# Kernel optimization log

Measured on AMD Instinct MI355X. Metric: run time of the kernel, lower is better.

## Reference

```python
import jax, jax.numpy as jnp
import numpy as np

N = 50000      # nodes
E = 1_600_000  # edges (avg degree 32)
IN, H, OUT, R = 128, 64, 32, 8
NEG_SLOPE = 0.2


def _rgat(x, src, dst, etype, W, q, k, b, n_nodes):
    """PyG RGATConv, defaults: heads=1, dim=1, additive-self-attention,
    across-relation softmax, concat=True, bias=True, dropout=0 (eval)."""
    # per-relation transform of all nodes: [R, N, O] (cheaper than per-edge bmm since 2*deg >> R)
    t = jnp.einsum('ni,rio->rno', x, W)
    xi = t[etype, dst]                      # [E, O] transformed target feats
    xj = t[etype, src]                      # [E, O] transformed source feats
    a = (xi @ q + xj @ k)[:, 0]             # [E] additive attention logits
    a = jnp.where(a >= 0, a, NEG_SLOPE * a)  # leaky_relu
    # segment softmax over incoming edges of each target node (across relations)
    m = jax.ops.segment_max(a, dst, num_segments=n_nodes)
    m = jnp.where(jnp.isfinite(m), m, 0.0)
    ex = jnp.exp(a - m[dst])
    s = jax.ops.segment_sum(ex, dst, num_segments=n_nodes)
    alpha = ex / (s[dst] + 1e-16)
    out = jax.ops.segment_sum(alpha[:, None] * xj, dst, num_segments=n_nodes)
    return out + b


def setup_inputs() -> dict:
    key = jax.random.key(0)
    ks = jax.random.split(key, 24)
    x = jax.random.normal(ks[0], (N, IN), jnp.float32)
    edge_index = jax.random.randint(ks[1], (2, E), 0, N, jnp.int32)
    edge_type = jax.random.randint(ks[2], (E,), 0, R, jnp.int32)

    def glorot(k, shape, fan_in):
        return jax.random.normal(k, shape, jnp.float32) * (1.0 / np.sqrt(fan_in))

    d = dict(x=x, edge_index=edge_index, edge_type=edge_type)
    # conv1: in->hidden, conv_mu / conv_logvar: hidden->hidden
    d['W1'] = glorot(ks[3], (R, IN, H), IN)
    d['q1'] = glorot(ks[4], (H, 1), H)
    d['k1'] = glorot(ks[5], (H, 1), H)
    d['b1'] = jnp.zeros((H,), jnp.float32)
    d['Wmu'] = glorot(ks[6], (R, H, H), H)
    d['qmu'] = glorot(ks[7], (H, 1), H)
    d['kmu'] = glorot(ks[8], (H, 1), H)
    d['bmu'] = jnp.zeros((H,), jnp.float32)
    d['Wlv'] = glorot(ks[9], (R, H, H), H)
    d['qlv'] = glorot(ks[10], (H, 1), H)
    d['klv'] = glorot(ks[11], (H, 1), H)
    d['blv'] = jnp.zeros((H,), jnp.float32)
    d['Wm'] = glorot(ks[12], (H, OUT), H)   # linear_mu (stored [in,out])
    d['bm'] = jnp.zeros((OUT,), jnp.float32)
    d['Wl'] = glorot(ks[13], (H, OUT), H)   # linear_logvar
    d['bl'] = jnp.zeros((OUT,), jnp.float32)
    return d


def reference(x, edge_index, edge_type, W1, q1, k1, b1,
              Wmu, qmu, kmu, bmu, Wlv, qlv, klv, blv, Wm, bm, Wl, bl):
    src, dst = edge_index[0], edge_index[1]
    hidden = jax.nn.relu(_rgat(x, src, dst, edge_type, W1, q1, k1, b1, N))
    mu = jax.nn.relu(_rgat(hidden, src, dst, edge_type, Wmu, qmu, kmu, bmu, N))
    mu = mu @ Wm + bm                       # dropout is identity in eval
    logvar = jax.nn.relu(_rgat(hidden, src, dst, edge_type, Wlv, qlv, klv, blv, N))
    logvar = logvar @ Wl + bl
    logstd = 0.5 * logvar
    return (mu, logstd)
```

## Files before the change

kernel.cpp:

```cpp
#include <hip/hip_runtime.h>
#include <cstdint>

#define HDIM 64
#define ODIM 32
#define NEG_SLOPE 0.2f
#define SCHUNK 2048
#define EPB 8192

typedef __attribute__((ext_vector_type(8))) short v8s;
typedef __attribute__((ext_vector_type(4))) float v4f;

__device__ __forceinline__ unsigned f2bf_rne(float f) {
  unsigned u = __float_as_uint(f);
  return (u + 0x7FFFu + ((u >> 16) & 1u)) >> 16;
}

__device__ __forceinline__ unsigned fenc(float f) {
  unsigned u = __float_as_uint(f);
  return (u & 0x80000000u) ? ~u : (u | 0x80000000u);
}
__device__ __forceinline__ float fdec(unsigned e) {
  unsigned u = (e & 0x80000000u) ? (e ^ 0x80000000u) : ~e;
  return __uint_as_float(u);
}

__global__ __launch_bounds__(256) void cvt_bf16_kernel(
    const float* __restrict__ in, unsigned short* __restrict__ out, int n) {
  int i = (blockIdx.x * 256 + threadIdx.x) * 4;
  if (i + 3 < n) {
    float4 v = *(const float4*)&in[i];
    ushort4 o;
    o.x = (unsigned short)f2bf_rne(v.x);
    o.y = (unsigned short)f2bf_rne(v.y);
    o.z = (unsigned short)f2bf_rne(v.z);
    o.w = (unsigned short)f2bf_rne(v.w);
    *(ushort4*)&out[i] = o;
  }
}

__global__ __launch_bounds__(256) void transpose_w_kernel(
    const float* __restrict__ W1, const float* __restrict__ Wmu,
    const float* __restrict__ Wlv, unsigned short* __restrict__ W1t,
    unsigned short* __restrict__ Wct) {
  const int b = blockIdx.x;
  if (b < 8) {
    const int r = b;
    for (int idx = threadIdx.x; idx < 128 * 64; idx += 256) {
      const int kk = idx >> 6, o = idx & 63;
      W1t[((size_t)r * 64 + o) * 128 + kk] =
          (unsigned short)f2bf_rne(W1[((size_t)r * 128 + kk) * 64 + o]);
    }
  } else {
    const int s = (b - 8) >> 3, r = (b - 8) & 7;
    const float* src = s ? Wlv : Wmu;
    for (int idx = threadIdx.x; idx < 64 * 64; idx += 256) {
      const int kk = idx >> 6, o = idx & 63;
      Wct[((size_t)s * 64 + o) * 512 + r * 64 + kk] =
          (unsigned short)f2bf_rne(src[((size_t)r * 64 + kk) * 64 + o]);
    }
  }
}

__global__ __launch_bounds__(256) void prep_T_kernel(
    const float* __restrict__ Wmu, const float* __restrict__ qmu,
    const float* __restrict__ kmu, const float* __restrict__ Wlv,
    const float* __restrict__ qlv, const float* __restrict__ klv,
    float* __restrict__ T) {
  for (int idx = threadIdx.x; idx < 2048; idx += 256) {
    const int j = idx >> 6, c = idx & 63;
    const int isk = j >> 4, sr = j & 15, s = sr >> 3, r = sr & 7;
    const float* W = s ? Wlv : Wmu;
    const float* vec = s ? (isk ? klv : qlv) : (isk ? kmu : qmu);
    float acc = 0.f;
    for (int o = 0; o < 64; o++)
      acc += W[((size_t)r * 64 + c) * 64 + o] * vec[o];
    T[idx] = acc;
  }
}

__global__ __launch_bounds__(256) void count_deg_kernel(
    const int* __restrict__ dst, const int* __restrict__ etype,
    int* __restrict__ deg, int E) {
  int e = blockIdx.x * 256 + threadIdx.x;
  if (e < E) atomicAdd(&deg[dst[e] * 8 + etype[e]], 1);
}

__global__ __launch_bounds__(256) void scan_p1(const int* __restrict__ deg,
                                               int* __restrict__ bsum, int n) {
  int base = blockIdx.x * SCHUNK + threadIdx.x * 8;
  int s = 0;
#pragma unroll
  for (int j = 0; j < 8; j++) {
    int i = base + j;
    if (i < n) s += deg[i];
  }
#pragma unroll
  for (int d = 1; d < 64; d <<= 1) s += __shfl_xor(s, d, 64);
  __shared__ int ws[4];
  if ((threadIdx.x & 63) == 0) ws[threadIdx.x >> 6] = s;
  __syncthreads();
  if (threadIdx.x == 0) bsum[blockIdx.x] = ws[0] + ws[1] + ws[2] + ws[3];
}

__global__ __launch_bounds__(256) void scan_p2(int* bsum, int nb) {
  __shared__ int wsum[4];
  const int i = threadIdx.x;
  int v = (i < nb) ? bsum[i] : 0;
  const int orig = v;
  const int lane = i & 63, w = i >> 6;
#pragma unroll
  for (int d = 1; d < 64; d <<= 1) {
    int up = __shfl_up(v, d, 64);
    if (lane >= d) v += up;
  }
  if (lane == 63) wsum[w] = v;
  __syncthreads();
  int woff = 0;
#pragma unroll
  for (int k = 0; k < 4; k++) woff += (k < w) ? wsum[k] : 0;
  if (i < nb) bsum[i] = woff + v - orig;
}

__global__ __launch_bounds__(256) void scan_p3(const int* __restrict__ deg,
                                               const int* __restrict__ bsum,
                                               int* __restrict__ row_ptr,
                                               int n) {
  int base = blockIdx.x * SCHUNK + threadIdx.x * 8;
  int vals[8];
  int s = 0;
#pragma unroll
  for (int j = 0; j < 8; j++) {
    int i = base + j;
    vals[j] = (i < n) ? deg[i] : 0;
    s += vals[j];
  }
  int lane = threadIdx.x & 63, w = threadIdx.x >> 6;
  int v = s;
#pragma unroll
  for (int d = 1; d < 64; d <<= 1) {
    int up = __shfl_up(v, d, 64);
    if (lane >= d) v += up;
  }
  __shared__ int wsum[4];
  if (lane == 63) wsum[w] = v;
  __syncthreads();
  int woff = 0;
#pragma unroll
  for (int i = 0; i < 4; i++) woff += (i < w) ? wsum[i] : 0;
  int off = bsum[blockIdx.x] + woff + v - s;
#pragma unroll
  for (int j = 0; j < 8; j++) {
    int i = base + j;
    off += vals[j];
    if (i < n) row_ptr[i + 1] = off;
  }
  if (blockIdx.x == 0 && threadIdx.x == 0) row_ptr[0] = 0;
}

__global__ __launch_bounds__(256) void bucket_cursor_init(
    const int* __restrict__ rp2, int* __restrict__ cursor, int N, int nb) {
  int i = threadIdx.x;
  if (i < nb) cursor[i] = rp2[(size_t)min(i * 256, N) * 8];
}

__global__ __launch_bounds__(256) void bucket_pass1(
    const int* __restrict__ src, const int* __restrict__ dst,
    const int* __restrict__ etype, int* __restrict__ cursor,
    unsigned* __restrict__ tmp, int E) {
  __shared__ int hist[256];
  __shared__ int binstart[256];
  __shared__ int gbase[256];
  __shared__ int fill[256];
  __shared__ int wsum[4];
  __shared__ unsigned stage[EPB];
  __shared__ unsigned char binof[EPB];
  const int tid = threadIdx.x;
  const int e0 = blockIdx.x * EPB;
  const int cnt = min(EPB, E - e0);

  hist[tid] = 0;
  fill[tid] = 0;
  __syncthreads();
  for (int j = tid; j < cnt; j += 256) atomicAdd(&hist[dst[e0 + j] >> 8], 1);
  __syncthreads();

  const int hv = hist[tid];
  {
    const int lane = tid & 63, w = tid >> 6;
    int iv = hv;
#pragma unroll
    for (int d = 1; d < 64; d <<= 1) {
      int up = __shfl_up(iv, d, 64);
      if (lane >= d) iv += up;
    }
    if (lane == 63) wsum[w] = iv;
    __syncthreads();
    int woff = 0;
#pragma unroll
    for (int i = 0; i < 4; i++) woff += (i < w) ? wsum[i] : 0;
    binstart[tid] = woff + iv - hv;
    if (hv > 0) gbase[tid] = atomicAdd(&cursor[tid], hv);
  }
  __syncthreads();

  for (int j = tid; j < cnt; j += 256) {
    const int d = dst[e0 + j];
    const int b = d >> 8;
    const unsigned rec = ((unsigned)(d & 255) << 19) |
                         ((unsigned)etype[e0 + j] << 16) |
                         (unsigned)src[e0 + j];
    const int slot = binstart[b] + atomicAdd(&fill[b], 1);
    stage[slot] = rec;
    binof[slot] = (unsigned char)b;
  }
  __syncthreads();

  for (int s = tid; s < cnt; s += 256) {
    const int b = binof[s];
    tmp[gbase[b] + (s - binstart[b])] = stage[s];
  }
}

__global__ __launch_bounds__(256) void bucket_pass2(
    const int* __restrict__ rp2, const unsigned* __restrict__ tmp,
    int* __restrict__ edges, int N) {
  __shared__ int rp[2049];
  __shared__ int fill[2048];
  const int tid = threadIdx.x;
  const int rowbase = blockIdx.x * 256;
  const int rowcnt = min(256, N - rowbase);
  for (int i = tid; i <= rowcnt * 8; i += 256) rp[i] = rp2[(size_t)rowbase * 8 + i];
  for (int i = tid; i < 2048; i += 256) fill[i] = 0;
  __syncthreads();
  const int beg = rp[0];
  const int endv = rp[rowcnt * 8];
  for (int i = beg + tid; i < endv; i += 256) {
    const unsigned rec = tmp[i];
    const int bin = rec >> 16;
    const int pos = rp[bin] + atomicAdd(&fill[bin], 1);
    edges[pos] = (int)(rec & 0x7FFFFu);
  }
}

__global__ __launch_bounds__(256) void rowmax_kernel(
    const float* __restrict__ ak, unsigned* __restrict__ maxk_enc, int N) {
  const int row = blockIdx.x;
  const int nchunks = gridDim.y;
  const int per = (N + nchunks - 1) / nchunks;
  const int beg = blockIdx.y * per;
  const int end = min(N, beg + per);
  const float* r = ak + (size_t)row * N;
  float m = -1e30f;
  for (int i = beg + threadIdx.x; i < end; i += 256) m = fmaxf(m, r[i]);
#pragma unroll
  for (int d = 1; d < 64; d <<= 1) m = fmaxf(m, __shfl_xor(m, d, 64));
  __shared__ float ws[4];
  if ((threadIdx.x & 63) == 0) ws[threadIdx.x >> 6] = m;
  __syncthreads();
  if (threadIdx.x == 0) {
    float bm = fmaxf(fmaxf(ws[0], ws[1]), fmaxf(ws[2], ws[3]));
    atomicMax(&maxk_enc[row], fenc(bm));
  }
}

__global__ __launch_bounds__(256) void transform1_mfma(
    const unsigned short* __restrict__ xb,
    const unsigned short* __restrict__ W1t, const float* __restrict__ q,
    const float* __restrict__ k, unsigned short* __restrict__ tb,
    float* __restrict__ aq, float* __restrict__ ak, int N) {
  __shared__ unsigned short st[4][16][72];
  const int r = blockIdx.x;
  const int tid = threadIdx.x;
  const int w = tid >> 6;
  const int lane = tid & 63;
  const int quad = lane >> 4;
  const int mrow = lane & 15;
  const int n0w = blockIdx.y * 64 + w * 16;

  const int gA = min(n0w + mrow, N - 1);
  const unsigned short* arow = xb + (size_t)gA * 128 + quad * 8;
  const unsigned short* wrow = W1t + ((size_t)r * 64 + mrow) * 128 + quad * 8;

  v4f acc[4];
#pragma unroll
  for (int tt = 0; tt < 4; tt++) acc[tt] = (v4f){0.f, 0.f, 0.f, 0.f};

#pragma unroll
  for (int k0 = 0; k0 < 128; k0 += 32) {
    v8s a = *(const v8s*)(arow + k0);
#pragma unroll
    for (int tt = 0; tt < 4; tt++) {
      v8s b = *(const v8s*)(wrow + (size_t)tt * 16 * 128 + k0);
      acc[tt] = __builtin_amdgcn_mfma_f32_16x16x32_bf16(a, b, acc[tt], 0, 0, 0);
    }
  }

  float qv[4], kv[4];
#pragma unroll
  for (int tt = 0; tt < 4; tt++) {
    qv[tt] = q[tt * 16 + mrow];
    kv[tt] = k[tt * 16 + mrow];
  }

#pragma unroll
  for (int i = 0; i < 4; i++) {
    float vq = 0.f, vk = 0.f;
#pragma unroll
    for (int tt = 0; tt < 4; tt++) {
      vq = fmaf(acc[tt][i], qv[tt], vq);
      vk = fmaf(acc[tt][i], kv[tt], vk);
      st[w][quad * 4 + i][tt * 16 + mrow] =
          (unsigned short)f2bf_rne(acc[tt][i]);
    }
#pragma unroll
    for (int d = 1; d < 16; d <<= 1) {
      vq += __shfl_xor(vq, d, 64);
      vk += __shfl_xor(vk, d, 64);
    }
    const int gn = n0w + quad * 4 + i;
    if (mrow == 0 && gn < N) {
      aq[(size_t)r * N + gn] = vq;
      ak[(size_t)r * N + gn] = vk;
    }
  }
  __syncthreads();

  const int row = lane >> 2, cg = lane & 3;
  const int gns = n0w + row;
  if (gns < N) {
    const uint4 v0 = *(const uint4*)&st[w][row][cg * 16];
    const uint4 v1 = *(const uint4*)&st[w][row][cg * 16 + 8];
    uint4* dst = (uint4*)&tb[((size_t)r * N + gns) * 64 + cg * 16];
    dst[0] = v0;
    dst[1] = v1;
  }
}

__global__ __launch_bounds__(256) void aggregate_kernel(
    const int* __restrict__ rp2, const int* __restrict__ edges,
    const unsigned short* __restrict__ tb, const float* __restrict__ aq,
    const float* __restrict__ ak, const unsigned* __restrict__ maxk_enc,
    const float* __restrict__ bias, unsigned short* __restrict__ hb, int N) {
  const int tid = threadIdx.x;
  const int w = tid >> 6, o = tid & 63;
  int wid = blockIdx.x * 4 + w;
  const bool valid = wid < N;
  if (!valid) wid = N - 1;
  const int beg = rp2[(size_t)wid * 8];
  const int end = valid ? rp2[(size_t)wid * 8 + 8] : beg;
  const int deg = end - beg;

  const float aqw = aq[(size_t)(o & 7) * N + wid];

  float v = aqw + fdec(maxk_enc[o & 7]);
  v = (v >= 0.f) ? v : NEG_SLOPE * v;
#pragma unroll
  for (int d = 1; d < 8; d <<= 1) v = fmaxf(v, __shfl_xor(v, d, 64));
  const float m = __shfl(v, 0, 64);

  const int g = o >> 3;
  const int cl = o & 7;
  float s = 0.f;
  float acc[8];
#pragma unroll
  for (int c = 0; c < 8; c++) acc[c] = 0.f;

  for (int base = 0; base < deg; base += 64) {
    const int j = base + o;
    const int gcount = min(64, deg - base);
    const int packed = edges[beg + min(j, deg - 1)];
    const int src = packed & 0xFFFF;
    const int rr = packed >> 16;
    const int idx = rr * N + src;
    float x = __shfl(aqw, rr, 64) + ak[idx];
    x = (x >= 0.f) ? x : NEG_SLOPE * x;
    const float p = (j < deg) ? __expf(x - m) : 0.f;
    s += p;
    const int g8 = (gcount + 7) & ~7;
    for (int u = 0; u < g8; u += 8) {
      const int e = u + g;
      const float pe = __shfl(p, e, 64);
      const int ie = __shfl(idx, e, 64);
      const uint4 tv = *(const uint4*)(tb + (size_t)ie * 64 + cl * 8);
      const unsigned uu0 = tv.x, uu1 = tv.y, uu2 = tv.z, uu3 = tv.w;
      acc[0] = fmaf(pe, __uint_as_float(uu0 << 16), acc[0]);
      acc[1] = fmaf(pe, __uint_as_float(uu0 & 0xFFFF0000u), acc[1]);
      acc[2] = fmaf(pe, __uint_as_float(uu1 << 16), acc[2]);
      acc[3] = fmaf(pe, __uint_as_float(uu1 & 0xFFFF0000u), acc[3]);
      acc[4] = fmaf(pe, __uint_as_float(uu2 << 16), acc[4]);
      acc[5] = fmaf(pe, __uint_as_float(uu2 & 0xFFFF0000u), acc[5]);
      acc[6] = fmaf(pe, __uint_as_float(uu3 << 16), acc[6]);
      acc[7] = fmaf(pe, __uint_as_float(uu3 & 0xFFFF0000u), acc[7]);
    }
  }
#pragma unroll
  for (int d = 1; d < 64; d <<= 1) s += __shfl_xor(s, d, 64);
#pragma unroll
  for (int d = 8; d < 64; d <<= 1) {
#pragma unroll
    for (int c = 0; c < 8; c++) acc[c] += __shfl_xor(acc[c], d, 64);
  }

  if (valid && g == 0) {
    const float inv = 1.f / (s + 1e-16f);
    unsigned rv[8];
#pragma unroll
    for (int c = 0; c < 8; c++) {
      const float res = acc[c] * inv + bias[cl * 8 + c];
      rv[c] = f2bf_rne(fmaxf(res, 0.f));
    }
    uint4 pkd;
    pkd.x = rv[0] | (rv[1] << 16);
    pkd.y = rv[2] | (rv[3] << 16);
    pkd.z = rv[4] | (rv[5] << 16);
    pkd.w = rv[6] | (rv[7] << 16);
    *(uint4*)(hb + (size_t)wid * 64 + cl * 8) = pkd;
  }
}

__global__ __launch_bounds__(256) void logit2_kernel(
    const unsigned short* __restrict__ hb, const float* __restrict__ T,
    float* __restrict__ aq2, float* __restrict__ ak2, int N) {
  __shared__ float Ts[2048];
  for (int i = threadIdx.x; i < 2048; i += 256) Ts[i] = T[i];
  __syncthreads();
  const int n = blockIdx.x * 256 + threadIdx.x;
  if (n >= N) return;
  float h[64];
  const unsigned short* hr = hb + (size_t)n * 64;
#pragma unroll
  for (int d = 0; d < 8; d++) {
    const uint4 u = *(const uint4*)(hr + d * 8);
    h[d * 8 + 0] = __uint_as_float(u.x << 16);
    h[d * 8 + 1] = __uint_as_float(u.x & 0xFFFF0000u);
    h[d * 8 + 2] = __uint_as_float(u.y << 16);
    h[d * 8 + 3] = __uint_as_float(u.y & 0xFFFF0000u);
    h[d * 8 + 4] = __uint_as_float(u.z << 16);
    h[d * 8 + 5] = __uint_as_float(u.z & 0xFFFF0000u);
    h[d * 8 + 6] = __uint_as_float(u.w << 16);
    h[d * 8 + 7] = __uint_as_float(u.w & 0xFFFF0000u);
  }
#pragma unroll
  for (int j = 0; j < 16; j++) {
    float dq = 0.f, dk = 0.f;
#pragma unroll
    for (int c = 0; c < 64; c++) {
      dq = fmaf(h[c], Ts[j * 64 + c], dq);
      dk = fmaf(h[c], Ts[(16 + j) * 64 + c], dk);
    }
    aq2[(size_t)j * N + n] = dq;
    ak2[(size_t)j * N + n] = dk;
  }
}

__global__ __launch_bounds__(256) void aggregate2h_kernel(
    const int* __restrict__ rp2, const int* __restrict__ edges,
    const unsigned short* __restrict__ hb, const float* __restrict__ aq2,
    const float* __restrict__ ak2, const unsigned* __restrict__ maxk2_enc,
    unsigned* __restrict__ y, float* __restrict__ sbuf, int N) {
  __shared__ float sred[2][2];
  const int tid = threadIdx.x;
  const int w = tid >> 6, o = tid & 63;
  const int nl = w >> 1;
  const int rbase = (w & 1) * 4;
  int wid = blockIdx.x * 2 + nl;
  const bool valid = wid < N;
  if (!valid) wid = N - 1;
  if (tid < 4) ((float*)sred)[tid] = 0.f;
  __syncthreads();

  const float aqw = aq2[(size_t)(o & 15) * N + wid];
  float v = aqw + fdec(maxk2_enc[o & 15]);
  v = (v >= 0.f) ? v : NEG_SLOPE * v;
#pragma unroll
  for (int d = 1; d < 8; d <<= 1) v = fmaxf(v, __shfl_xor(v, d, 64));
  const float m0 = __shfl(v, 0, 64);
  const float m1 = __shfl(v, 8, 64);

  const int g = o >> 5;
  const int k = o & 31;
  float s0 = 0.f, s1 = 0.f;
  float aE0[4], aO0[4], aE1[4], aO1[4];
#pragma unroll
  for (int r = 0; r < 4; r++) {
    aE0[r] = 0.f;
    aO0[r] = 0.f;
    aE1[r] = 0.f;
    aO1[r] = 0.f;
  }

  const size_t segbase = (size_t)wid * 8 + rbase;
#pragma unroll
  for (int r = 0; r < 4; r++) {
    const int sb = rp2[segbase + r];
    const int se = rp2[segbase + r + 1];
    if (valid && sb < se) {
      const float aqr0 = __shfl(aqw, rbase + r, 64);
      const float aqr1 = __shfl(aqw, 8 + rbase + r, 64);
      for (int base = sb; base < se; base += 64) {
        const int j = base + o;
        const int cnt = min(64, se - base);
        const int src = edges[min(j, se - 1)] & 0xFFFF;
        const float akv0 = ak2[(size_t)(rbase + r) * N + src];
        const float akv1 = ak2[(size_t)(8 + rbase + r) * N + src];
        float x0 = aqr0 + akv0;
        float x1 = aqr1 + akv1;
        x0 = (x0 >= 0.f) ? x0 : NEG_SLOPE * x0;
        x1 = (x1 >= 0.f) ? x1 : NEG_SLOPE * x1;
        const float p0 = (j < se) ? __expf(x0 - m0) : 0.f;
        const float p1 = (j < se) ? __expf(x1 - m1) : 0.f;
        s0 += p0;
        s1 += p1;
        for (int u = 0; 2 * u < cnt; u++) {
          const int e = 2 * u + g;
          const float pe0 = __shfl(p0, e, 64);
          const float pe1 = __shfl(p1, e, 64);
          const int ie = __shfl(src, e, 64);
          const unsigned hw =
              *(const unsigned*)(hb + (size_t)ie * 64 + k * 2);
          const float h0 = __uint_as_float(hw << 16);
          const float h1 = __uint_as_float(hw & 0xFFFF0000u);
          aE0[r] = fmaf(pe0, h0, aE0[r]);
          aO0[r] = fmaf(pe0, h1, aO0[r]);
          aE1[r] = fmaf(pe1, h0, aE1[r]);
          aO1[r] = fmaf(pe1, h1, aO1[r]);
        }
      }
    }
  }

#pragma unroll
  for (int d = 1; d < 64; d <<= 1) {
    s0 += __shfl_xor(s0, d, 64);
    s1 += __shfl_xor(s1, d, 64);
  }
#pragma unroll
  for (int r = 0; r < 4; r++) {
    aE0[r] += __shfl_xor(aE0[r], 32, 64);
    aO0[r] += __shfl_xor(aO0[r], 32, 64);
    aE1[r] += __shfl_xor(aE1[r], 32, 64);
    aO1[r] += __shfl_xor(aO1[r], 32, 64);
  }
  if (valid && o == 0) {
    atomicAdd(&sred[nl][0], s0);
    atomicAdd(&sred[nl][1], s1);
  }
  if (valid && g == 0) {
#pragma unroll
    for (int r = 0; r < 4; r++) {
      const unsigned u0 = f2bf_rne(aE0[r]) | (f2bf_rne(aO0[r]) << 16);
      const unsigned u1 = f2bf_rne(aE1[r]) | (f2bf_rne(aO1[r]) << 16);
      y[(size_t)wid * 256 + (rbase + r) * 32 + k] = u0;
      y[((size_t)N + wid) * 256 + (rbase + r) * 32 + k] = u1;
    }
  }
  __syncthreads();
  if (valid && o == 0 && rbase == 0) {
    sbuf[(size_t)wid * 2 + 0] = sred[nl][0];
    sbuf[(size_t)wid * 2 + 1] = sred[nl][1];
  }
}

__global__ __launch_bounds__(256) void out2_kernel(
    const unsigned short* __restrict__ yb,
    const unsigned short* __restrict__ Wct, const float* __restrict__ sbuf,
    const float* __restrict__ bmu, const float* __restrict__ blv,
    const float* __restrict__ Wm, const float* __restrict__ bm,
    const float* __restrict__ Wl, const float* __restrict__ bl,
    float* __restrict__ out_mu, float* __restrict__ out_ls, int N) {
  __shared__ float hstf[64][65];
  __shared__ float WL[2048];
  __shared__ float b2L[32];
  const int s = blockIdx.y;
  const int tid = threadIdx.x;
  for (int i = tid; i < 2048; i += 256) WL[i] = s ? Wl[i] : Wm[i];
  if (tid < 32) b2L[tid] = s ? bl[tid] : bm[tid];

  const int w = tid >> 6, lane = tid & 63;
  const int quad = lane >> 4, mrow = lane & 15;
  const int n0w = blockIdx.x * 64 + w * 16;
  const int gA = min(n0w + mrow, N - 1);
  const unsigned short* arow = yb + ((size_t)s * N + gA) * 512 + quad * 8;
  const unsigned short* wrow = Wct + ((size_t)s * 64 + mrow) * 512 + quad * 8;

  v4f acc[4];
#pragma unroll
  for (int tt = 0; tt < 4; tt++) acc[tt] = (v4f){0.f, 0.f, 0.f, 0.f};
#pragma unroll
  for (int k0 = 0; k0 < 512; k0 += 32) {
    v8s a = *(const v8s*)(arow + k0);
#pragma unroll
    for (int tt = 0; tt < 4; tt++) {
      v8s b = *(const v8s*)(wrow + (size_t)tt * 16 * 512 + k0);
      acc[tt] = __builtin_amdgcn_mfma_f32_16x16x32_bf16(a, b, acc[tt], 0, 0, 0);
    }
  }

  const float* bc = s ? blv : bmu;
#pragma unroll
  for (int i = 0; i < 4; i++) {
    const int node = min(n0w + quad * 4 + i, N - 1);
    const float inv = 1.f / (sbuf[(size_t)node * 2 + s] + 1e-16f);
#pragma unroll
    for (int tt = 0; tt < 4; tt++) {
      hstf[w * 16 + quad * 4 + i][tt * 16 + mrow] =
          fmaxf(acc[tt][i] * inv + bc[tt * 16 + mrow], 0.f);
    }
  }
  __syncthreads();

  const float mul = s ? 0.5f : 1.f;
  float* outp = s ? out_ls : out_mu;
  for (int idx = tid; idx < 2048; idx += 256) {
    const int nl2 = idx >> 5, oo = idx & 31;
    const int node = blockIdx.x * 64 + nl2;
    float a2 = 0.f;
#pragma unroll
    for (int c = 0; c < 64; c++) a2 = fmaf(hstf[nl2][c], WL[c * 32 + oo], a2);
    if (node < N) outp[(size_t)node * 32 + oo] = (a2 + b2L[oo]) * mul;
  }
}

extern "C" void kernel_launch(void* const* d_in, const int* in_sizes, int n_in,
                              void* d_out, int out_size, void* d_ws,
                              size_t ws_size, hipStream_t stream) {
  const float* x = (const float*)d_in[0];
  const int* edge_index = (const int*)d_in[1];
  const int* edge_type = (const int*)d_in[2];
  const float* W1 = (const float*)d_in[3];
  const float* q1 = (const float*)d_in[4];
  const float* k1 = (const float*)d_in[5];
  const float* b1 = (const float*)d_in[6];
  const float* Wmu = (const float*)d_in[7];
  const float* qmu = (const float*)d_in[8];
  const float* kmu = (const float*)d_in[9];
  const float* bmu = (const float*)d_in[10];
  const float* Wlv = (const float*)d_in[11];
  const float* qlv = (const float*)d_in[12];
  const float* klv = (const float*)d_in[13];
  const float* blv = (const float*)d_in[14];
  const float* Wm = (const float*)d_in[15];
  const float* bm = (const float*)d_in[16];
  const float* Wl = (const float*)d_in[17];
  const float* bl = (const float*)d_in[18];

  const int N = in_sizes[0] / 128;
  const int E = in_sizes[2];
  const int R = in_sizes[3] / (128 * 64);

  float* out_mu = (float*)d_out;
  float* out_ls = (float*)d_out + (size_t)N * ODIM;

  char* wsp = (char*)d_ws;
  size_t off = 0;
  auto carve = [&](size_t bytes) {
    void* p = wsp + off;
    off += (bytes + 255) & ~(size_t)255;
    return p;
  };

  void* tbuf = carve((size_t)R * N * 64 * sizeof(unsigned));
  unsigned short* t1b = (unsigned short*)tbuf;
  unsigned short* yb = (unsigned short*)tbuf;
  unsigned* yw = (unsigned*)tbuf;
  unsigned short* xb = (unsigned short*)carve((size_t)N * 128 * 2);
  unsigned short* hb = (unsigned short*)carve((size_t)N * 64 * 2);
  unsigned short* W1t = (unsigned short*)carve((size_t)R * 64 * 128 * 2);
  unsigned short* Wct = (unsigned short*)carve((size_t)2 * 64 * 512 * 2);
  float* Tdir = (float*)carve((size_t)32 * 64 * sizeof(float));
  float* aq2 = (float*)carve((size_t)2 * R * N * sizeof(float));
  float* ak2 = (float*)carve((size_t)2 * R * N * sizeof(float));
  unsigned* maxk_enc = (unsigned*)carve(2 * R * sizeof(unsigned));
  float* sbuf = (float*)carve((size_t)N * 2 * sizeof(float));
  int* deg = (int*)carve((size_t)N * 8 * sizeof(int));
  int* rp2 = (int*)carve(((size_t)N * 8 + 1) * sizeof(int));
  int* bsum = (int*)carve(256 * sizeof(int));
  int* cursor = (int*)carve(256 * sizeof(int));
  unsigned* tmp = (unsigned*)carve((size_t)E * sizeof(unsigned));
  int* edges = (int*)carve((size_t)E * sizeof(int));

  const int* e_src = edge_index;
  const int* e_dst = edge_index + E;

  cvt_bf16_kernel<<<(N * 128 / 4 + 255) / 256, 256, 0, stream>>>(x, xb,
                                                                 N * 128);
  transpose_w_kernel<<<24, 256, 0, stream>>>(W1, Wmu, Wlv, W1t, Wct);
  prep_T_kernel<<<1, 256, 0, stream>>>(Wmu, qmu, kmu, Wlv, qlv, klv, Tdir);

  hipMemsetAsync(deg, 0, (size_t)N * 8 * sizeof(int), stream);
  hipMemsetAsync(maxk_enc, 0, 2 * R * sizeof(unsigned), stream);
  count_deg_kernel<<<(E + 255) / 256, 256, 0, stream>>>(e_dst, edge_type, deg,
                                                        E);
  const int n2 = N * 8;
  const int nchunk = (n2 + SCHUNK - 1) / SCHUNK;
  scan_p1<<<nchunk, 256, 0, stream>>>(deg, bsum, n2);
  scan_p2<<<1, 256, 0, stream>>>(bsum, nchunk);
  scan_p3<<<nchunk, 256, 0, stream>>>(deg, bsum, rp2, n2);

  const int nbuck = (N + 255) >> 8;
  bucket_cursor_init<<<1, 256, 0, stream>>>(rp2, cursor, N, nbuck);
  bucket_pass1<<<(E + EPB - 1) / EPB, 256, 0, stream>>>(e_src, e_dst,
                                                        edge_type, cursor,
                                                        tmp, E);
  bucket_pass2<<<nbuck, 256, 0, stream>>>(rp2, tmp, edges, N);

  const int nb64 = (N + 63) / 64;

  transform1_mfma<<<dim3(R, nb64), 256, 0, stream>>>(xb, W1t, q1, k1, t1b,
                                                     aq2, ak2, N);
  rowmax_kernel<<<dim3(R, 32), 256, 0, stream>>>(ak2, maxk_enc, N);
  aggregate_kernel<<<(N + 3) / 4, 256, 0, stream>>>(rp2, edges, t1b, aq2, ak2,
                                                    maxk_enc, b1, hb, N);

  logit2_kernel<<<(N + 255) / 256, 256, 0, stream>>>(hb, Tdir, aq2, ak2, N);
  hipMemsetAsync(maxk_enc, 0, 2 * R * sizeof(unsigned), stream);
  rowmax_kernel<<<dim3(2 * R, 32), 256, 0, stream>>>(ak2, maxk_enc, N);
  aggregate2h_kernel<<<(N + 1) / 2, 256, 0, stream>>>(rp2, edges, hb, aq2,
                                                      ak2, maxk_enc, yw, sbuf,
                                                      N);
  out2_kernel<<<dim3(nb64, 2), 256, 0, stream>>>(yb, Wct, sbuf, bmu, blv, Wm,
                                                 bm, Wl, bl, out_mu, out_ls,
                                                 N);
}
```

Measured before the change: 609.4 us.

## Fuse per-relation key max into producers and restructure layer-2 aggregation per relation

Removes the two rowmax kernels and one memset by computing the per-relation max of key logits inside transform1 and logit2, combined across blocks with atomicMax on an encoded float. The layer-2 aggregation is rewritten so each wave handles one node, with 8 lanes per relation segment walking edges serially. Each lane loads 16 bytes of the source row and keeps 8-wide accumulators, which replaces the old shuffle-broadcast loop and the shared-memory reduction. The serial per-segment loop exposes load latency per edge and leaves lanes idle when relation degrees are uneven, in exchange for fewer shuffles, no block syncs and wider loads.

```diff
diff --git a/kernel.cpp b/kernel.cpp
--- a/kernel.cpp
+++ b/kernel.cpp
@@ -229,7 +229,8 @@
   const int tid = threadIdx.x;
   const int rowbase = blockIdx.x * 256;
   const int rowcnt = min(256, N - rowbase);
-  for (int i = tid; i <= rowcnt * 8; i += 256) rp[i] = rp2[(size_t)rowbase * 8 + i];
+  for (int i = tid; i <= rowcnt * 8; i += 256)
+    rp[i] = rp2[(size_t)rowbase * 8 + i];
   for (int i = tid; i < 2048; i += 256) fill[i] = 0;
   __syncthreads();
   const int beg = rp[0];
@@ -242,33 +243,14 @@
   }
 }
 
-__global__ __launch_bounds__(256) void rowmax_kernel(
-    const float* __restrict__ ak, unsigned* __restrict__ maxk_enc, int N) {
-  const int row = blockIdx.x;
-  const int nchunks = gridDim.y;
-  const int per = (N + nchunks - 1) / nchunks;
-  const int beg = blockIdx.y * per;
-  const int end = min(N, beg + per);
-  const float* r = ak + (size_t)row * N;
-  float m = -1e30f;
-  for (int i = beg + threadIdx.x; i < end; i += 256) m = fmaxf(m, r[i]);
-#pragma unroll
-  for (int d = 1; d < 64; d <<= 1) m = fmaxf(m, __shfl_xor(m, d, 64));
-  __shared__ float ws[4];
-  if ((threadIdx.x & 63) == 0) ws[threadIdx.x >> 6] = m;
-  __syncthreads();
-  if (threadIdx.x == 0) {
-    float bm = fmaxf(fmaxf(ws[0], ws[1]), fmaxf(ws[2], ws[3]));
-    atomicMax(&maxk_enc[row], fenc(bm));
-  }
-}
-
 __global__ __launch_bounds__(256) void transform1_mfma(
     const unsigned short* __restrict__ xb,
     const unsigned short* __restrict__ W1t, const float* __restrict__ q,
     const float* __restrict__ k, unsigned short* __restrict__ tb,
-    float* __restrict__ aq, float* __restrict__ ak, int N) {
+    float* __restrict__ aq, float* __restrict__ ak,
+    unsigned* __restrict__ maxk_enc, int N) {
   __shared__ unsigned short st[4][16][72];
+  __shared__ float wsm[4];
   const int r = blockIdx.x;
   const int tid = threadIdx.x;
   const int w = tid >> 6;
@@ -302,6 +284,7 @@
     kv[tt] = k[tt * 16 + mrow];
   }
 
+  float kmax = -1e30f;
 #pragma unroll
   for (int i = 0; i < 4; i++) {
     float vq = 0.f, vk = 0.f;
@@ -317,13 +300,21 @@
       vq += __shfl_xor(vq, d, 64);
       vk += __shfl_xor(vk, d, 64);
     }
+    kmax = fmaxf(kmax, vk);
     const int gn = n0w + quad * 4 + i;
     if (mrow == 0 && gn < N) {
       aq[(size_t)r * N + gn] = vq;
       ak[(size_t)r * N + gn] = vk;
     }
   }
-  __syncthreads();
+#pragma unroll
+  for (int d = 1; d < 64; d <<= 1) kmax = fmaxf(kmax, __shfl_xor(kmax, d, 64));
+  if (lane == 0) wsm[w] = kmax;
+  __syncthreads();
+  if (tid == 0) {
+    atomicMax(&maxk_enc[r],
+              fenc(fmaxf(fmaxf(wsm[0], wsm[1]), fmaxf(wsm[2], wsm[3]))));
+  }
 
   const int row = lane >> 2, cg = lane & 3;
   const int gns = n0w + row;
@@ -420,12 +411,15 @@
 
 __global__ __launch_bounds__(256) void logit2_kernel(
     const unsigned short* __restrict__ hb, const float* __restrict__ T,
-    float* __restrict__ aq2, float* __restrict__ ak2, int N) {
+    float* __restrict__ aq2, float* __restrict__ ak2,
+    unsigned* __restrict__ maxk2_enc, int N) {
   __shared__ float Ts[2048];
+  __shared__ float wred[4][16];
   for (int i = threadIdx.x; i < 2048; i += 256) Ts[i] = T[i];
   __syncthreads();
-  const int n = blockIdx.x * 256 + threadIdx.x;
-  if (n >= N) return;
+  const int n0 = blockIdx.x * 256 + threadIdx.x;
+  const bool valid = n0 < N;
+  const int n = valid ? n0 : N - 1;
   float h[64];
   const unsigned short* hr = hb + (size_t)n * 64;
 #pragma unroll
@@ -440,6 +434,7 @@
     h[d * 8 + 6] = __uint_as_float(u.w << 16);
     h[d * 8 + 7] = __uint_as_float(u.w & 0xFFFF0000u);
   }
+  float kmx[16];
 #pragma unroll
   for (int j = 0; j < 16; j++) {
     float dq = 0.f, dk = 0.f;
@@ -448,26 +443,38 @@
       dq = fmaf(h[c], Ts[j * 64 + c], dq);
       dk = fmaf(h[c], Ts[(16 + j) * 64 + c], dk);
     }
-    aq2[(size_t)j * N + n] = dq;
-    ak2[(size_t)j * N + n] = dk;
-  }
-}
-
-__global__ __launch_bounds__(256) void aggregate2h_kernel(
+    if (valid) {
+      aq2[(size_t)j * N + n] = dq;
+      ak2[(size_t)j * N + n] = dk;
+    }
+    kmx[j] = dk;
+  }
+  const int lane = threadIdx.x & 63, w = threadIdx.x >> 6;
+#pragma unroll
+  for (int j = 0; j < 16; j++) {
+#pragma unroll
+    for (int d = 1; d < 64; d <<= 1)
+      kmx[j] = fmaxf(kmx[j], __shfl_xor(kmx[j], d, 64));
+    if (lane == 0) wred[w][j] = kmx[j];
+  }
+  __syncthreads();
+  if (threadIdx.x < 16) {
+    const float bm = fmaxf(fmaxf(wred[0][threadIdx.x], wred[1][threadIdx.x]),
+                           fmaxf(wred[2][threadIdx.x], wred[3][threadIdx.x]));
+    atomicMax(&maxk2_enc[threadIdx.x], fenc(bm));
+  }
+}
+
+__global__ __launch_bounds__(256) void aggregate2g_kernel(
     const int* __restrict__ rp2, const int* __restrict__ edges,
     const unsigned short* __restrict__ hb, const float* __restrict__ aq2,
     const float* __restrict__ ak2, const unsigned* __restrict__ maxk2_enc,
     unsigned* __restrict__ y, float* __restrict__ sbuf, int N) {
-  __shared__ float sred[2][2];
   const int tid = threadIdx.x;
   const int w = tid >> 6, o = tid & 63;
-  const int nl = w >> 1;
-  const int rbase = (w & 1) * 4;
-  int wid = blockIdx.x * 2 + nl;
+  int wid = blockIdx.x * 4 + w;
   const bool valid = wid < N;
   if (!valid) wid = N - 1;
-  if (tid < 4) ((float*)sred)[tid] = 0.f;
-  __syncthreads();
 
   const float aqw = aq2[(size_t)(o & 15) * N + wid];
   float v = aqw + fdec(maxk2_enc[o & 15]);
@@ -477,87 +484,86 @@
   const float m0 = __shfl(v, 0, 64);
   const float m1 = __shfl(v, 8, 64);
 
-  const int g = o >> 5;
-  const int k = o & 31;
+  const int grp = o >> 3;
+  const int ln = o & 7;
+  const float aqr0 = __shfl(aqw, grp, 64);
+  const float aqr1 = __shfl(aqw, 8 + grp, 64);
+
+  const int sb = rp2[(size_t)wid * 8 + grp];
+  const int se = rp2[(size_t)wid * 8 + grp + 1];
+
+  float acc0[8], acc1[8];
+#pragma unroll
+  for (int c = 0; c < 8; c++) {
+    acc0[c] = 0.f;
+    acc1[c] = 0.f;
+  }
   float s0 = 0.f, s1 = 0.f;
-  float aE0[4], aO0[4], aE1[4], aO1[4];
-#pragma unroll
-  for (int r = 0; r < 4; r++) {
-    aE0[r] = 0.f;
-    aO0[r] = 0.f;
-    aE1[r] = 0.f;
-    aO1[r] = 0.f;
-  }
-
-  const size_t segbase = (size_t)wid * 8 + rbase;
-#pragma unroll
-  for (int r = 0; r < 4; r++) {
-    const int sb = rp2[segbase + r];
-    const int se = rp2[segbase + r + 1];
-    if (valid && sb < se) {
-      const float aqr0 = __shfl(aqw, rbase + r, 64);
-      const float aqr1 = __shfl(aqw, 8 + rbase + r, 64);
-      for (int base = sb; base < se; base += 64) {
-        const int j = base + o;
-        const int cnt = min(64, se - base);
-        const int src = edges[min(j, se - 1)] & 0xFFFF;
-        const float akv0 = ak2[(size_t)(rbase + r) * N + src];
-        const float akv1 = ak2[(size_t)(8 + rbase + r) * N + src];
-        float x0 = aqr0 + akv0;
-        float x1 = aqr1 + akv1;
-        x0 = (x0 >= 0.f) ? x0 : NEG_SLOPE * x0;
-        x1 = (x1 >= 0.f) ? x1 : NEG_SLOPE * x1;
-        const float p0 = (j < se) ? __expf(x0 - m0) : 0.f;
-        const float p1 = (j < se) ? __expf(x1 - m1) : 0.f;
-        s0 += p0;
-        s1 += p1;
-        for (int u = 0; 2 * u < cnt; u++) {
-          const int e = 2 * u + g;
-          const float pe0 = __shfl(p0, e, 64);
-          const float pe1 = __shfl(p1, e, 64);
-          const int ie = __shfl(src, e, 64);
-          const unsigned hw =
-              *(const unsigned*)(hb + (size_t)ie * 64 + k * 2);
-          const float h0 = __uint_as_float(hw << 16);
-          const float h1 = __uint_as_float(hw & 0xFFFF0000u);
-          aE0[r] = fmaf(pe0, h0, aE0[r]);
-          aO0[r] = fmaf(pe0, h1, aO0[r]);
-          aE1[r] = fmaf(pe1, h0, aE1[r]);
-          aO1[r] = fmaf(pe1, h1, aO1[r]);
-        }
-      }
-    }
-  }
-
-#pragma unroll
-  for (int d = 1; d < 64; d <<= 1) {
+
+  const size_t akoff0 = (size_t)grp * N;
+  const size_t akoff1 = (size_t)(8 + grp) * N;
+  for (int e = sb; e < se; ++e) {
+    const int src = edges[e] & 0xFFFF;
+    const float akv0 = ak2[akoff0 + src];
+    const float akv1 = ak2[akoff1 + src];
+    const uint4 hv = *(const uint4*)(hb + (size_t)src * 64 + ln * 8);
+    float x0 = aqr0 + akv0;
+    float x1 = aqr1 + akv1;
+    x0 = (x0 >= 0.f) ? x0 : NEG_SLOPE * x0;
+    x1 = (x1 >= 0.f) ? x1 : NEG_SLOPE * x1;
+    const float p0 = __expf(x0 - m0);
+    const float p1 = __expf(x1 - m1);
+    s0 += p0;
+    s1 += p1;
+    const unsigned uu0 = hv.x, uu1 = hv.y, uu2 = hv.z, uu3 = hv.w;
+    const float h0 = __uint_as_float(uu0 << 16);
+    const float h1 = __uint_as_float(uu0 & 0xFFFF0000u);
+    const float h2 = __uint_as_float(uu1 << 16);
+    const float h3 = __uint_as_float(uu1 & 0xFFFF0000u);
+    const float h4 = __uint_as_float(uu2 << 16);
+    const float h5 = __uint_as_float(uu2 & 0xFFFF0000u);
+    const float h6 = __uint_as_float(uu3 << 16);
+    const float h7 = __uint_as_float(uu3 & 0xFFFF0000u);
+    acc0[0] = fmaf(p0, h0, acc0[0]);
+    acc0[1] = fmaf(p0, h1, acc0[1]);
+    acc0[2] = fmaf(p0, h2, acc0[2]);
+    acc0[3] = fmaf(p0, h3, acc0[3]);
+    acc0[4] = fmaf(p0, h4, acc0[4]);
+    acc0[5] = fmaf(p0, h5, acc0[5]);
+    acc0[6] = fmaf(p0, h6, acc0[6]);
+    acc0[7] = fmaf(p0, h7, acc0[7]);
+    acc1[0] = fmaf(p1, h0, acc1[0]);
+    acc1[1] = fmaf(p1, h1, acc1[1]);
+    acc1[2] = fmaf(p1, h2, acc1[2]);
+    acc1[3] = fmaf(p1, h3, acc1[3]);
+    acc1[4] = fmaf(p1, h4, acc1[4]);
+    acc1[5] = fmaf(p1, h5, acc1[5]);
+    acc1[6] = fmaf(p1, h6, acc1[6]);
+    acc1[7] = fmaf(p1, h7, acc1[7]);
+  }
+
+  if (valid) {
+    uint4 p0w, p1w;
+    p0w.x = f2bf_rne(acc0[0]) | (f2bf_rne(acc0[1]) << 16);
+    p0w.y = f2bf_rne(acc0[2]) | (f2bf_rne(acc0[3]) << 16);
+    p0w.z = f2bf_rne(acc0[4]) | (f2bf_rne(acc0[5]) << 16);
+    p0w.w = f2bf_rne(acc0[6]) | (f2bf_rne(acc0[7]) << 16);
+    p1w.x = f2bf_rne(acc1[0]) | (f2bf_rne(acc1[1]) << 16);
+    p1w.y = f2bf_rne(acc1[2]) | (f2bf_rne(acc1[3]) << 16);
+    p1w.z = f2bf_rne(acc1[4]) | (f2bf_rne(acc1[5]) << 16);
+    p1w.w = f2bf_rne(acc1[6]) | (f2bf_rne(acc1[7]) << 16);
+    *(uint4*)(y + (size_t)wid * 256 + 4 * o) = p0w;
+    *(uint4*)(y + ((size_t)N + wid) * 256 + 4 * o) = p1w;
+  }
+
+#pragma unroll
+  for (int d = 8; d < 64; d <<= 1) {
     s0 += __shfl_xor(s0, d, 64);
     s1 += __shfl_xor(s1, d, 64);
   }
-#pragma unroll
-  for (int r = 0; r < 4; r++) {
-    aE0[r] += __shfl_xor(aE0[r], 32, 64);
-    aO0[r] += __shfl_xor(aO0[r], 32, 64);
-    aE1[r] += __shfl_xor(aE1[r], 32, 64);
-    aO1[r] += __shfl_xor(aO1[r], 32, 64);
-  }
   if (valid && o == 0) {
-    atomicAdd(&sred[nl][0], s0);
-    atomicAdd(&sred[nl][1], s1);
-  }
-  if (valid && g == 0) {
-#pragma unroll
-    for (int r = 0; r < 4; r++) {
-      const unsigned u0 = f2bf_rne(aE0[r]) | (f2bf_rne(aO0[r]) << 16);
-      const unsigned u1 = f2bf_rne(aE1[r]) | (f2bf_rne(aO1[r]) << 16);
-      y[(size_t)wid * 256 + (rbase + r) * 32 + k] = u0;
-      y[((size_t)N + wid) * 256 + (rbase + r) * 32 + k] = u1;
-    }
-  }
-  __syncthreads();
-  if (valid && o == 0 && rbase == 0) {
-    sbuf[(size_t)wid * 2 + 0] = sred[nl][0];
-    sbuf[(size_t)wid * 2 + 1] = sred[nl][1];
+    sbuf[(size_t)wid * 2 + 0] = s0;
+    sbuf[(size_t)wid * 2 + 1] = s1;
   }
 }
 
@@ -670,7 +676,7 @@
   float* Tdir = (float*)carve((size_t)32 * 64 * sizeof(float));
   float* aq2 = (float*)carve((size_t)2 * R * N * sizeof(float));
   float* ak2 = (float*)carve((size_t)2 * R * N * sizeof(float));
-  unsigned* maxk_enc = (unsigned*)carve(2 * R * sizeof(unsigned));
+  unsigned* maxk_enc = (unsigned*)carve(32 * sizeof(unsigned));
   float* sbuf = (float*)carve((size_t)N * 2 * sizeof(float));
   int* deg = (int*)carve((size_t)N * 8 * sizeof(int));
   int* rp2 = (int*)carve(((size_t)N * 8 + 1) * sizeof(int));
@@ -688,7 +694,7 @@
   prep_T_kernel<<<1, 256, 0, stream>>>(Wmu, qmu, kmu, Wlv, qlv, klv, Tdir);
 
   hipMemsetAsync(deg, 0, (size_t)N * 8 * sizeof(int), stream);
-  hipMemsetAsync(maxk_enc, 0, 2 * R * sizeof(unsigned), stream);
+  hipMemsetAsync(maxk_enc, 0, 32 * sizeof(unsigned), stream);
   count_deg_kernel<<<(E + 255) / 256, 256, 0, stream>>>(e_dst, edge_type, deg,
                                                         E);
   const int n2 = N * 8;
@@ -705,19 +711,17 @@
   bucket_pass2<<<nbuck, 256, 0, stream>>>(rp2, tmp, edges, N);
 
   const int nb64 = (N + 63) / 64;
+  const int agg_blocks = (N + 3) / 4;
 
   transform1_mfma<<<dim3(R, nb64), 256, 0, stream>>>(xb, W1t, q1, k1, t1b,
-                                                     aq2, ak2, N);
-  rowmax_kernel<<<dim3(R, 32), 256, 0, stream>>>(ak2, maxk_enc, N);
-  aggregate_kernel<<<(N + 3) / 4, 256, 0, stream>>>(rp2, edges, t1b, aq2, ak2,
-                                                    maxk_enc, b1, hb, N);
-
-  logit2_kernel<<<(N + 255) / 256, 256, 0, stream>>>(hb, Tdir, aq2, ak2, N);
-  hipMemsetAsync(maxk_enc, 0, 2 * R * sizeof(unsigned), stream);
-  rowmax_kernel<<<dim3(2 * R, 32), 256, 0, stream>>>(ak2, maxk_enc, N);
-  aggregate2h_kernel<<<(N + 1) / 2, 256, 0, stream>>>(rp2, edges, hb, aq2,
-                                                      ak2, maxk_enc, yw, sbuf,
-                                                      N);
+                                                     aq2, ak2, maxk_enc, N);
+  aggregate_kernel<<<agg_blocks, 256, 0, stream>>>(rp2, edges, t1b, aq2, ak2,
+                                                   maxk_enc, b1, hb, N);
+
+  logit2_kernel<<<(N + 255) / 256, 256, 0, stream>>>(hb, Tdir, aq2, ak2,
+                                                     maxk_enc + 8, N);
+  aggregate2g_kernel<<<agg_blocks, 256, 0, stream>>>(
+      rp2, edges, hb, aq2, ak2, maxk_enc + 8, yw, sbuf, N);
   out2_kernel<<<dim3(nb64, 2), 256, 0, stream>>>(yb, Wct, sbuf, bmu, blv, Wm,
                                                  bm, Wl, bl, out_mu, out_ls,
                                                  N);
```

Result: faster. 559.0 us (-8.3%).
